# Performance work log

Hardware: AMD Instinct MI355X
Metric: run time of the kernel (lower is better)

Reference implementation:

```python
import jax, jax.numpy as jnp
import numpy as np

B, T, D = 4, 4096, 1024
EPS = 1e-5  # FusedRMSNormSwishGate default eps


def setup_inputs() -> dict:
    key = jax.random.key(0)
    ks = jax.random.split(key, 6)
    s = 1.0 / np.sqrt(D)
    return {
        "x": jax.random.normal(ks[0], (B, T, D), jnp.float32),
        "Wi": jax.random.normal(ks[1], (D, D), jnp.float32) * s,
        "Wf": jax.random.normal(ks[2], (D, D), jnp.float32) * s,
        "Wg": jax.random.normal(ks[3], (D, D), jnp.float32) * s,
        "Wo": jax.random.normal(ks[4], (D, D), jnp.float32) * s,
        "norm_w": jnp.ones((D,), jnp.float32),
    }


def _hgrn_scan(f, i):
    # h_t = f_t * h_{t-1} + i_t  (elementwise gated linear recurrence)
    # associative combine: (f1,i1) o (f2,i2) = (f1*f2, i1*f2 + i2)
    def combine(a, b):
        fa, ia = a
        fb, ib = b
        return fa * fb, ia * fb + ib

    _, h = jax.lax.associative_scan(combine, (f, i), axis=1)
    return h


def reference(x, Wi, Wf, Wg, Wo, norm_w):
    # projections
    i = x @ Wi.T                                  # [B,T,D]
    f = jax.nn.sigmoid(x @ Wf.T)                  # forget gate in (0,1)
    # swiglu(i, 1-f): silu on the value, gated by the input gate (1-f)
    inp = jax.nn.silu(i) * (1.0 - f)
    # hierarchically-gated linear recurrence (chunk/parallel scan form)
    h = _hgrn_scan(f, inp)                        # [B,T,D]
    # RMSNorm(h) * swish(g) output gate
    g = x @ Wg.T
    rms = h * jax.lax.rsqrt(jnp.mean(h * h, axis=-1, keepdims=True) + EPS)
    o = (rms * norm_w) * (g * jax.nn.sigmoid(g))
    return o @ Wo.T
```

## Files before the change

kernel.cpp:

```cpp
#include <hip/hip_runtime.h>
#include <hip/hip_bf16.h>

typedef unsigned short u16;
using bf16x8 = __bf16 __attribute__((ext_vector_type(8)));
using f32x4  = float  __attribute__((ext_vector_type(4)));

#define BB 4
#define TT 4096
#define DD 1024
#define MROWS (BB*TT)
#define CT 64
#define NC (TT/CT)

__device__ __forceinline__ float sigm(float x) { return 1.0f / (1.0f + __expf(-x)); }
__device__ __forceinline__ u16 f2bf(float f) {
    __hip_bfloat16 h = __float2bfloat16(f);
    return *reinterpret_cast<u16*>(&h);
}
__device__ __forceinline__ float bf2f(u16 u) { return __uint_as_float(((unsigned)u) << 16); }

__device__ __forceinline__ void async_cp16(const u16* g, u16* l) {
    __builtin_amdgcn_global_load_lds(
        (const __attribute__((address_space(1))) unsigned int*)g,
        (__attribute__((address_space(3))) unsigned int*)l, 16, 0, 0);
}

__global__ __launch_bounds__(256) void conv_x_kernel(const float* __restrict__ s,
                                                     u16* __restrict__ d) {
    size_t i = (size_t)blockIdx.x * 256 + threadIdx.x;
    float4 v = *(const float4*)(s + i * 4);
    ushort4 u;
    u.x = f2bf(v.x); u.y = f2bf(v.y); u.z = f2bf(v.z); u.w = f2bf(v.w);
    *(ushort4*)(d + i * 4) = u;
}

__global__ __launch_bounds__(256) void conv_w4_kernel(const float* __restrict__ w0,
                                                      const float* __restrict__ w1,
                                                      const float* __restrict__ w2,
                                                      const float* __restrict__ w3,
                                                      u16* __restrict__ dst) {
    int i = blockIdx.x * 256 + threadIdx.x;
    int sel = i >> 18;
    int off = i & 262143;
    const float* s = (sel == 0) ? w0 : (sel == 1) ? w1 : (sel == 2) ? w2 : w3;
    float4 v = *(const float4*)(s + (size_t)off * 4);
    ushort4 u;
    u.x = f2bf(v.x); u.y = f2bf(v.y); u.z = f2bf(v.z); u.w = f2bf(v.w);
    *(ushort4*)(dst + ((size_t)sel << 20) + (size_t)off * 4) = u;
}

#define BM 128
#define BN 128
#define BK 64

template <typename OutT>
__global__ __launch_bounds__(256, 2)
void gemm_bf16_bt(const u16* __restrict__ Ag, const u16* __restrict__ Bg, int K,
                  OutT* __restrict__ P0, OutT* __restrict__ P1, OutT* __restrict__ P2) {
    __shared__ u16 As[BM * BK];
    __shared__ u16 Bs[BN * BK];

    const int tid  = threadIdx.x;
    const int lane = tid & 63;
    const int wid  = tid >> 6;
    const int wm   = wid >> 1;
    const int wn   = wid & 1;
    const int lr   = lane & 15;
    const int lq   = lane >> 4;

    const long bM  = (long)blockIdx.y * BM;
    const long bN0 = (long)blockIdx.x * BN;

    const f32x4 zero = {0.f, 0.f, 0.f, 0.f};
    f32x4 acc[4][4];
#pragma unroll
    for (int i = 0; i < 4; i++)
#pragma unroll
        for (int j = 0; j < 4; j++) acc[i][j] = zero;

    for (int kt = 0; kt < K; kt += BK) {
        __syncthreads();
#pragma unroll
        for (int j = 0; j < 4; j++) {
            const int G  = j * 256 + tid;
            const int m  = G >> 3;
            const int p  = G & 7;
            const int gk = p ^ (m & 7);
            async_cp16(Ag + (bM + m) * K + kt + gk * 8, &As[G * 8]);
            async_cp16(Bg + (bN0 + m) * K + kt + gk * 8, &Bs[G * 8]);
        }
        __syncthreads();
#pragma unroll
        for (int kk = 0; kk < BK / 32; kk++) {
            bf16x8 av[4], bv[4];
#pragma unroll
            for (int f = 0; f < 4; f++) {
                const int am = wm * 64 + f * 16 + lr;
                const int ag = (kk * 4 + lq) ^ (am & 7);
                av[f] = *(const bf16x8*)(&As[am * 64 + ag * 8]);
                const int bn = wn * 64 + f * 16 + lr;
                const int bg = (kk * 4 + lq) ^ (bn & 7);
                bv[f] = *(const bf16x8*)(&Bs[bn * 64 + bg * 8]);
            }
#pragma unroll
            for (int i = 0; i < 4; i++)
#pragma unroll
                for (int j = 0; j < 4; j++)
                    acc[i][j] = __builtin_amdgcn_mfma_f32_16x16x32_bf16(av[i], bv[j],
                                                                        acc[i][j], 0, 0, 0);
        }
    }

    const int pl = (int)(bN0 >> 10);
    OutT* P = (pl == 0) ? P0 : ((pl == 1) ? P1 : P2);
    const int cn = (int)(bN0 & 1023);
#pragma unroll
    for (int i = 0; i < 4; i++) {
        const long m0 = bM + wm * 64 + i * 16 + lq * 4;
#pragma unroll
        for (int j = 0; j < 4; j++) {
            const int n = cn + wn * 64 + j * 16 + lr;
#pragma unroll
            for (int r = 0; r < 4; r++) {
                if constexpr (sizeof(OutT) == 2)
                    P[(m0 + r) * 1024 + n] = f2bf(acc[i][j][r]);
                else
                    P[(m0 + r) * 1024 + n] = acc[i][j][r];
            }
        }
    }
}

__global__ __launch_bounds__(256) void scan_pass1(const u16* __restrict__ ip,
                                                  const u16* __restrict__ fp,
                                                  float* __restrict__ Fc,
                                                  float* __restrict__ Ic) {
    const int tid = blockIdx.x * 256 + threadIdx.x;
    const int d4  = tid & 255;
    const int c   = (tid >> 8) & (NC - 1);
    const int b   = tid >> 14;
    size_t base = ((size_t)(b * TT + c * CT) << 10) + (size_t)d4 * 4;
    float F[4] = {1.f, 1.f, 1.f, 1.f};
    float I[4] = {0.f, 0.f, 0.f, 0.f};
#pragma unroll 8
    for (int t = 0; t < CT; t++) {
        ushort4 fu = *(const ushort4*)(fp + base);
        ushort4 iu = *(const ushort4*)(ip + base);
        base += DD;
        const u16 fa[4] = {fu.x, fu.y, fu.z, fu.w};
        const u16 ia[4] = {iu.x, iu.y, iu.z, iu.w};
#pragma unroll
        for (int j = 0; j < 4; j++) {
            float f  = sigm(bf2f(fa[j]));
            float iv = bf2f(ia[j]);
            float v  = iv * sigm(iv) * (1.f - f);
            I[j] = fmaf(f, I[j], v);
            F[j] *= f;
        }
    }
    const size_t o = (((size_t)(b * NC + c)) << 10) + (size_t)d4 * 4;
    float4 vF = {F[0], F[1], F[2], F[3]};
    float4 vI = {I[0], I[1], I[2], I[3]};
    *(float4*)(Fc + o) = vF;
    *(float4*)(Ic + o) = vI;
}

__global__ __launch_bounds__(256) void scan_pass2(const float* __restrict__ Fc,
                                                  const float* __restrict__ Ic,
                                                  float* __restrict__ Hin) {
    const int gtid = blockIdx.x * 256 + threadIdx.x;
    const int lane = gtid & 63;
    const int w    = gtid >> 6;
    const int b    = w >> 10;
    const int d    = w & 1023;
    const int idx  = ((b * NC + lane) << 10) + d;
    float F = Fc[idx];
    float I = Ic[idx];
#pragma unroll
    for (int s = 1; s < 64; s <<= 1) {
        float Fp = __shfl_up(F, s, 64);
        float Ip = __shfl_up(I, s, 64);
        if (lane >= s) {
            I = fmaf(Ip, F, I);
            F *= Fp;
        }
    }
    float Hex = __shfl_up(I, 1, 64);
    if (lane == 0) Hex = 0.f;
    Hin[idx] = Hex;
}

__global__ __launch_bounds__(256) void scan_pass3(const u16* __restrict__ ip,
                                                  const u16* __restrict__ fp,
                                                  const float* __restrict__ Hin,
                                                  u16* __restrict__ hout) {
    const int tid = blockIdx.x * 256 + threadIdx.x;
    const int d4  = tid & 255;
    const int c   = (tid >> 8) & (NC - 1);
    const int b   = tid >> 14;
    size_t base = ((size_t)(b * TT + c * CT) << 10) + (size_t)d4 * 4;
    const size_t o = (((size_t)(b * NC + c)) << 10) + (size_t)d4 * 4;
    float4 hv = *(const float4*)(Hin + o);
    float h[4] = {hv.x, hv.y, hv.z, hv.w};
#pragma unroll 8
    for (int t = 0; t < CT; t++) {
        ushort4 fu = *(const ushort4*)(fp + base);
        ushort4 iu = *(const ushort4*)(ip + base);
        const u16 fa[4] = {fu.x, fu.y, fu.z, fu.w};
        const u16 ia[4] = {iu.x, iu.y, iu.z, iu.w};
        ushort4 ou;
        u16 oa[4];
#pragma unroll
        for (int j = 0; j < 4; j++) {
            float f  = sigm(bf2f(fa[j]));
            float iv = bf2f(ia[j]);
            float v  = iv * sigm(iv) * (1.f - f);
            h[j] = fmaf(f, h[j], v);
            oa[j] = f2bf(h[j]);
        }
        ou.x = oa[0]; ou.y = oa[1]; ou.z = oa[2]; ou.w = oa[3];
        *(ushort4*)(hout + base) = ou;
        base += DD;
    }
}

__global__ __launch_bounds__(256) void rmsnorm_gate(const u16* hin,
                                                    const u16* __restrict__ g,
                                                    const float* __restrict__ w,
                                                    u16* oout) {
    const int row = blockIdx.x;
    const int t = threadIdx.x;
    const size_t base = ((size_t)row << 10) + t * 4;
    ushort4 hu = *(const ushort4*)(hin + base);
    float h0 = bf2f(hu.x), h1 = bf2f(hu.y), h2 = bf2f(hu.z), h3 = bf2f(hu.w);
    float ss = h0 * h0 + h1 * h1 + h2 * h2 + h3 * h3;
#pragma unroll
    for (int o = 32; o > 0; o >>= 1) ss += __shfl_down(ss, o);
    __shared__ float red[4];
    if ((t & 63) == 0) red[t >> 6] = ss;
    __syncthreads();
    const float tot = red[0] + red[1] + red[2] + red[3];
    const float rms = rsqrtf(tot * (1.f / 1024.f) + 1e-5f);
    ushort4 gu = *(const ushort4*)(g + base);
    float g0 = bf2f(gu.x), g1 = bf2f(gu.y), g2 = bf2f(gu.z), g3 = bf2f(gu.w);
    float4 wv = *(const float4*)(w + (size_t)t * 4);
    ushort4 ou;
    ou.x = f2bf(h0 * rms * wv.x * g0 * sigm(g0));
    ou.y = f2bf(h1 * rms * wv.y * g1 * sigm(g1));
    ou.z = f2bf(h2 * rms * wv.z * g2 * sigm(g2));
    ou.w = f2bf(h3 * rms * wv.w * g3 * sigm(g3));
    *(ushort4*)(oout + base) = ou;
}

extern "C" void kernel_launch(void* const* d_in, const int* in_sizes, int n_in,
                              void* d_out, int out_size, void* d_ws, size_t ws_size,
                              hipStream_t stream) {
    const float* x  = (const float*)d_in[0];
    const float* Wi = (const float*)d_in[1];
    const float* Wf = (const float*)d_in[2];
    const float* Wg = (const float*)d_in[3];
    const float* Wo = (const float*)d_in[4];
    const float* nw = (const float*)d_in[5];
    float* out = (float*)d_out;

    const size_t MB = 1ull << 20;
    char* ws = (char*)d_ws;
    u16*   xo  = (u16*)(ws);
    u16*   Wb  = (u16*)(ws + 32 * MB);
    u16*   Pi  = (u16*)(ws + 40 * MB);
    u16*   Pf  = (u16*)(ws + 72 * MB);
    float* Fc  = (float*)(ws + 104 * MB);
    float* Ic  = Fc + BB * NC * DD;
    float* Hin = Ic + BB * NC * DD;
    u16*   g   = (u16*)d_out;

    conv_x_kernel<<<16384, 256, 0, stream>>>(x, xo);
    conv_w4_kernel<<<4096, 256, 0, stream>>>(Wi, Wf, Wg, Wo, Wb);
    gemm_bf16_bt<u16><<<dim3(24, 128), 256, 0, stream>>>(xo, Wb, 1024, Pi, Pf, g);
    scan_pass1<<<256, 256, 0, stream>>>(Pi, Pf, Fc, Ic);
    scan_pass2<<<1024, 256, 0, stream>>>(Fc, Ic, Hin);
    scan_pass3<<<256, 256, 0, stream>>>(Pi, Pf, Hin, xo);
    rmsnorm_gate<<<16384, 256, 0, stream>>>(xo, g, nw, xo);
    gemm_bf16_bt<float><<<dim3(8, 128), 256, 0, stream>>>(xo, Wb + 3ull * 1024 * 1024, 1024,
                                                          out, out, out);
}
```

Before: 382.6 us.

## Replace GEMM with 256x256-tile double-buffered pipelined kernel

Measured after the change: 382.2 us. No clear change (-0.1%).

```diff
diff --git a/kernel.cpp b/kernel.cpp
--- a/kernel.cpp
+++ b/kernel.cpp
@@ -49,74 +49,126 @@
     *(ushort4*)(dst + ((size_t)sel << 20) + (size_t)off * 4) = u;
 }
 
-#define BM 128
-#define BN 128
-#define BK 64
+#define G_BM 256
+#define G_BN 256
+#define G_BK 64
+
+#define READ_A(dst, MH)                                                         \
+  { const u16* Ab = &As[(p * 2 + (MH)) << 13];                                  \
+    _Pragma("unroll") for (int kk = 0; kk < 2; kk++) {                          \
+      const int gsw = (((kk * 4 + lq) ^ lr7) << 3);                             \
+      _Pragma("unroll") for (int f = 0; f < 4; f++)                             \
+        dst[f][kk] = *(const bf16x8*)(Ab + (wm * 64 + f * 16 + lr) * 64 + gsw); \
+    } }
+#define READ_B(dst, NH)                                                         \
+  { const u16* Bb = &Bs[(p * 2 + (NH)) << 13];                                  \
+    _Pragma("unroll") for (int kk = 0; kk < 2; kk++) {                          \
+      const int gsw = (((kk * 4 + lq) ^ lr7) << 3);                             \
+      _Pragma("unroll") for (int j = 0; j < 2; j++)                             \
+        dst[j][kk] = *(const bf16x8*)(Bb + (wn * 32 + j * 16 + lr) * 64 + gsw); \
+    } }
+#define MFMA16(AV, BV, MH, NH)                                                  \
+  { _Pragma("unroll") for (int kk = 0; kk < 2; kk++)                            \
+    _Pragma("unroll") for (int f = 0; f < 4; f++)                               \
+    _Pragma("unroll") for (int j = 0; j < 2; j++)                               \
+      acc[(MH)*4+f][(NH)*2+j] = __builtin_amdgcn_mfma_f32_16x16x32_bf16(        \
+          AV[f][kk], BV[j][kk], acc[(MH)*4+f][(NH)*2+j], 0, 0, 0); }
+#define SYNC_PRE()                                                              \
+  do { __builtin_amdgcn_s_barrier();                                            \
+       asm volatile("s_waitcnt lgkmcnt(0)" ::: "memory");                       \
+       __builtin_amdgcn_s_setprio(1); } while (0)
+#define SYNC_POST()                                                             \
+  do { __builtin_amdgcn_s_setprio(0);                                           \
+       __builtin_amdgcn_s_barrier(); } while (0)
 
 template <typename OutT>
-__global__ __launch_bounds__(256, 2)
-void gemm_bf16_bt(const u16* __restrict__ Ag, const u16* __restrict__ Bg, int K,
-                  OutT* __restrict__ P0, OutT* __restrict__ P1, OutT* __restrict__ P2) {
-    __shared__ u16 As[BM * BK];
-    __shared__ u16 Bs[BN * BK];
+__global__ __launch_bounds__(512, 2)
+void gemm256(const u16* __restrict__ Ag, const u16* __restrict__ Bg, int K,
+             OutT* __restrict__ P0, OutT* __restrict__ P1, OutT* __restrict__ P2) {
+    __shared__ u16 As[32768];
+    __shared__ u16 Bs[32768];
 
     const int tid  = threadIdx.x;
     const int lane = tid & 63;
     const int wid  = tid >> 6;
-    const int wm   = wid >> 1;
-    const int wn   = wid & 1;
+    const int wm   = wid >> 2;
+    const int wn   = wid & 3;
     const int lr   = lane & 15;
     const int lq   = lane >> 4;
-
-    const long bM  = (long)blockIdx.y * BM;
-    const long bN0 = (long)blockIdx.x * BN;
+    const int lr7  = lr & 7;
+
+    const long bM  = (long)blockIdx.y * G_BM;
+    const long bN0 = (long)blockIdx.x * G_BN;
+    const int  KT  = K >> 6;
+
+    auto stageA = [&](int cc, int h) {
+#pragma unroll
+        for (int l = 0; l < 2; l++) {
+            const int G  = l * 512 + tid;
+            const int rl = G >> 3;
+            const int gk = (G & 7) ^ (rl & 7);
+            const int r  = (rl & 63) + h * 64 + ((rl >> 6) << 7);
+            async_cp16(Ag + (bM + r) * K + cc * 64 + gk * 8,
+                       &As[(((cc & 1) * 2 + h) << 13) + G * 8]);
+        }
+    };
+    auto stageB = [&](int cc, int h) {
+#pragma unroll
+        for (int l = 0; l < 2; l++) {
+            const int G  = l * 512 + tid;
+            const int rl = G >> 3;
+            const int gk = (G & 7) ^ (rl & 7);
+            const int r  = (rl & 31) + h * 32 + ((rl >> 5) << 6);
+            async_cp16(Bg + (bN0 + r) * K + cc * 64 + gk * 8,
+                       &Bs[(((cc & 1) * 2 + h) << 13) + G * 8]);
+        }
+    };
 
     const f32x4 zero = {0.f, 0.f, 0.f, 0.f};
-    f32x4 acc[4][4];
-#pragma unroll
-    for (int i = 0; i < 4; i++)
+    f32x4 acc[8][4];
+#pragma unroll
+    for (int i = 0; i < 8; i++)
 #pragma unroll
         for (int j = 0; j < 4; j++) acc[i][j] = zero;
 
-    for (int kt = 0; kt < K; kt += BK) {
-        __syncthreads();
-#pragma unroll
-        for (int j = 0; j < 4; j++) {
-            const int G  = j * 256 + tid;
-            const int m  = G >> 3;
-            const int p  = G & 7;
-            const int gk = p ^ (m & 7);
-            async_cp16(Ag + (bM + m) * K + kt + gk * 8, &As[G * 8]);
-            async_cp16(Bg + (bN0 + m) * K + kt + gk * 8, &Bs[G * 8]);
-        }
-        __syncthreads();
-#pragma unroll
-        for (int kk = 0; kk < BK / 32; kk++) {
-            bf16x8 av[4], bv[4];
-#pragma unroll
-            for (int f = 0; f < 4; f++) {
-                const int am = wm * 64 + f * 16 + lr;
-                const int ag = (kk * 4 + lq) ^ (am & 7);
-                av[f] = *(const bf16x8*)(&As[am * 64 + ag * 8]);
-                const int bn = wn * 64 + f * 16 + lr;
-                const int bg = (kk * 4 + lq) ^ (bn & 7);
-                bv[f] = *(const bf16x8*)(&Bs[bn * 64 + bg * 8]);
-            }
-#pragma unroll
-            for (int i = 0; i < 4; i++)
-#pragma unroll
-                for (int j = 0; j < 4; j++)
-                    acc[i][j] = __builtin_amdgcn_mfma_f32_16x16x32_bf16(av[i], bv[j],
-                                                                        acc[i][j], 0, 0, 0);
-        }
+    stageA(0, 0); stageB(0, 0); stageA(0, 1); stageB(0, 1);
+    if (KT > 1) {
+        stageA(1, 0); stageB(1, 0);
+        asm volatile("s_waitcnt vmcnt(4)" ::: "memory");
+    } else {
+        asm volatile("s_waitcnt vmcnt(0)" ::: "memory");
+    }
+    __builtin_amdgcn_s_barrier();
+
+    for (int c = 0; c < KT; ++c) {
+        const int  p  = c & 1;
+        const bool s1 = (c + 1 < KT);
+        const bool s2 = (c + 2 < KT);
+        bf16x8 av0[4][2], av1[4][2], bv0[2][2], bv1[2][2];
+        READ_A(av0, 0); READ_B(bv0, 0);
+        if (s1) stageA(c + 1, 1);
+        SYNC_PRE(); MFMA16(av0, bv0, 0, 0); SYNC_POST();
+        READ_B(bv1, 1);
+        if (s1) stageB(c + 1, 1);
+        SYNC_PRE(); MFMA16(av0, bv1, 0, 1); SYNC_POST();
+        READ_A(av1, 1);
+        if (s2) stageA(c + 2, 0);
+        SYNC_PRE(); MFMA16(av1, bv0, 1, 0); SYNC_POST();
+        if (s2) {
+            stageB(c + 2, 0);
+            asm volatile("s_waitcnt vmcnt(4)" ::: "memory");
+        } else if (s1) {
+            asm volatile("s_waitcnt vmcnt(0)" ::: "memory");
+        }
+        SYNC_PRE(); MFMA16(av1, bv1, 1, 1); SYNC_POST();
     }
 
     const int pl = (int)(bN0 >> 10);
     OutT* P = (pl == 0) ? P0 : ((pl == 1) ? P1 : P2);
     const int cn = (int)(bN0 & 1023);
 #pragma unroll
-    for (int i = 0; i < 4; i++) {
-        const long m0 = bM + wm * 64 + i * 16 + lq * 4;
+    for (int i = 0; i < 8; i++) {
+        const long m0 = bM + wm * 128 + i * 16 + lq * 4;
 #pragma unroll
         for (int j = 0; j < 4; j++) {
             const int n = cn + wn * 64 + j * 16 + lr;
@@ -276,11 +328,11 @@
 
     conv_x_kernel<<<16384, 256, 0, stream>>>(x, xo);
     conv_w4_kernel<<<4096, 256, 0, stream>>>(Wi, Wf, Wg, Wo, Wb);
-    gemm_bf16_bt<u16><<<dim3(24, 128), 256, 0, stream>>>(xo, Wb, 1024, Pi, Pf, g);
+    gemm256<u16><<<dim3(12, 64), 512, 0, stream>>>(xo, Wb, 1024, Pi, Pf, g);
     scan_pass1<<<256, 256, 0, stream>>>(Pi, Pf, Fc, Ic);
     scan_pass2<<<1024, 256, 0, stream>>>(Fc, Ic, Hin);
     scan_pass3<<<256, 256, 0, stream>>>(Pi, Pf, Hin, xo);
     rmsnorm_gate<<<16384, 256, 0, stream>>>(xo, g, nw, xo);
-    gemm_bf16_bt<float><<<dim3(8, 128), 256, 0, stream>>>(xo, Wb + 3ull * 1024 * 1024, 1024,
-                                                          out, out, out);
-}
+    gemm256<float><<<dim3(4, 64), 512, 0, stream>>>(xo, Wb + 3ull * 1024 * 1024, 1024,
+                                                    out, out, out);
+}
```

## Fuse RMSNorm-gate into scan pass3 and swizzle GEMM workgroup order

Applied to the files above, without the earlier changes.

Result: slower. 414.9 us (+8.4%).

```diff
diff --git a/kernel.cpp b/kernel.cpp
--- a/kernel.cpp
+++ b/kernel.cpp
@@ -68,8 +68,15 @@
     const int lr   = lane & 15;
     const int lq   = lane >> 4;
 
-    const long bM  = (long)blockIdx.y * BM;
-    const long bN0 = (long)blockIdx.x * BN;
+    const int nwg  = gridDim.x * gridDim.y;
+    const int flat = blockIdx.y * gridDim.x + blockIdx.x;
+    const int cpx  = nwg >> 3;
+    const int swz  = (flat & 7) * cpx + (flat >> 3);
+    const int bx   = swz % gridDim.x;
+    const int by   = swz / gridDim.x;
+
+    const long bM  = (long)by * BM;
+    const long bN0 = (long)bx * BN;
 
     const f32x4 zero = {0.f, 0.f, 0.f, 0.f};
     f32x4 acc[4][4];
@@ -190,66 +197,55 @@
     Hin[idx] = Hex;
 }
 
-__global__ __launch_bounds__(256) void scan_pass3(const u16* __restrict__ ip,
-                                                  const u16* __restrict__ fp,
-                                                  const float* __restrict__ Hin,
-                                                  u16* __restrict__ hout) {
-    const int tid = blockIdx.x * 256 + threadIdx.x;
-    const int d4  = tid & 255;
-    const int c   = (tid >> 8) & (NC - 1);
-    const int b   = tid >> 14;
-    size_t base = ((size_t)(b * TT + c * CT) << 10) + (size_t)d4 * 4;
-    const size_t o = (((size_t)(b * NC + c)) << 10) + (size_t)d4 * 4;
+__global__ __launch_bounds__(256) void scan_pass3_norm(const u16* __restrict__ ip,
+                                                       const u16* __restrict__ fp,
+                                                       const float* __restrict__ Hin,
+                                                       const u16* __restrict__ gp,
+                                                       const float* __restrict__ w,
+                                                       u16* __restrict__ oout) {
+    const int t_ = threadIdx.x;
+    const int c  = blockIdx.x & (NC - 1);
+    const int b  = blockIdx.x >> 6;
+    size_t base = ((size_t)(b * TT + c * CT) << 10) + (size_t)t_ * 4;
+    const size_t o = (((size_t)(b * NC + c)) << 10) + (size_t)t_ * 4;
     float4 hv = *(const float4*)(Hin + o);
     float h[4] = {hv.x, hv.y, hv.z, hv.w};
-#pragma unroll 8
+    const float4 wv = *(const float4*)(w + (size_t)t_ * 4);
+    const float wl[4] = {wv.x, wv.y, wv.z, wv.w};
+    __shared__ float red[2][4];
     for (int t = 0; t < CT; t++) {
         ushort4 fu = *(const ushort4*)(fp + base);
         ushort4 iu = *(const ushort4*)(ip + base);
+        ushort4 gu = *(const ushort4*)(gp + base);
         const u16 fa[4] = {fu.x, fu.y, fu.z, fu.w};
         const u16 ia[4] = {iu.x, iu.y, iu.z, iu.w};
-        ushort4 ou;
-        u16 oa[4];
+        const u16 ga[4] = {gu.x, gu.y, gu.z, gu.w};
+        float ss = 0.f;
 #pragma unroll
         for (int j = 0; j < 4; j++) {
             float f  = sigm(bf2f(fa[j]));
             float iv = bf2f(ia[j]);
             float v  = iv * sigm(iv) * (1.f - f);
             h[j] = fmaf(f, h[j], v);
-            oa[j] = f2bf(h[j]);
+            ss = fmaf(h[j], h[j], ss);
+        }
+#pragma unroll
+        for (int off = 32; off > 0; off >>= 1) ss += __shfl_down(ss, off);
+        if ((t_ & 63) == 0) red[t & 1][t_ >> 6] = ss;
+        __syncthreads();
+        const float tot = red[t & 1][0] + red[t & 1][1] + red[t & 1][2] + red[t & 1][3];
+        const float rms = rsqrtf(tot * (1.f / 1024.f) + 1e-5f);
+        ushort4 ou;
+        u16 oa[4];
+#pragma unroll
+        for (int j = 0; j < 4; j++) {
+            float gv = bf2f(ga[j]);
+            oa[j] = f2bf(h[j] * rms * wl[j] * gv * sigm(gv));
         }
         ou.x = oa[0]; ou.y = oa[1]; ou.z = oa[2]; ou.w = oa[3];
-        *(ushort4*)(hout + base) = ou;
+        *(ushort4*)(oout + base) = ou;
         base += DD;
     }
-}
-
-__global__ __launch_bounds__(256) void rmsnorm_gate(const u16* hin,
-                                                    const u16* __restrict__ g,
-                                                    const float* __restrict__ w,
-                                                    u16* oout) {
-    const int row = blockIdx.x;
-    const int t = threadIdx.x;
-    const size_t base = ((size_t)row << 10) + t * 4;
-    ushort4 hu = *(const ushort4*)(hin + base);
-    float h0 = bf2f(hu.x), h1 = bf2f(hu.y), h2 = bf2f(hu.z), h3 = bf2f(hu.w);
-    float ss = h0 * h0 + h1 * h1 + h2 * h2 + h3 * h3;
-#pragma unroll
-    for (int o = 32; o > 0; o >>= 1) ss += __shfl_down(ss, o);
-    __shared__ float red[4];
-    if ((t & 63) == 0) red[t >> 6] = ss;
-    __syncthreads();
-    const float tot = red[0] + red[1] + red[2] + red[3];
-    const float rms = rsqrtf(tot * (1.f / 1024.f) + 1e-5f);
-    ushort4 gu = *(const ushort4*)(g + base);
-    float g0 = bf2f(gu.x), g1 = bf2f(gu.y), g2 = bf2f(gu.z), g3 = bf2f(gu.w);
-    float4 wv = *(const float4*)(w + (size_t)t * 4);
-    ushort4 ou;
-    ou.x = f2bf(h0 * rms * wv.x * g0 * sigm(g0));
-    ou.y = f2bf(h1 * rms * wv.y * g1 * sigm(g1));
-    ou.z = f2bf(h2 * rms * wv.z * g2 * sigm(g2));
-    ou.w = f2bf(h3 * rms * wv.w * g3 * sigm(g3));
-    *(ushort4*)(oout + base) = ou;
 }
 
 extern "C" void kernel_launch(void* const* d_in, const int* in_sizes, int n_in,
@@ -279,8 +275,7 @@
     gemm_bf16_bt<u16><<<dim3(24, 128), 256, 0, stream>>>(xo, Wb, 1024, Pi, Pf, g);
     scan_pass1<<<256, 256, 0, stream>>>(Pi, Pf, Fc, Ic);
     scan_pass2<<<1024, 256, 0, stream>>>(Fc, Ic, Hin);
-    scan_pass3<<<256, 256, 0, stream>>>(Pi, Pf, Hin, xo);
-    rmsnorm_gate<<<16384, 256, 0, stream>>>(xo, g, nw, xo);
+    scan_pass3_norm<<<256, 256, 0, stream>>>(Pi, Pf, Hin, g, nw, xo);
     gemm_bf16_bt<float><<<dim3(8, 128), 256, 0, stream>>>(xo, Wb + 3ull * 1024 * 1024, 1024,
                                                           out, out, out);
 }
```
